# Kernel optimization log

Hardware: AMD Instinct MI355X
Metric: run time of the kernel (lower is better)

## Reference

```python
import jax, jax.numpy as jnp
import numpy as np

N_NODES = 50000
N_EDGES = 800000
HEADS = 4
OUT_CH = 64
NEG_SLOPE = 0.2  # PyG GATConv default


def gat_conv(x, edge_index, W, att_src, att_dst, bias):
    """PyG GATConv (concat=True, add_self_loops=True, eval mode).
    x: [N, F_in], edge_index: [2, E] (row 0 = src, row 1 = dst).
    W: [F_in, H*C], att_src/att_dst: [1, H, C], bias: [H*C].
    """
    n = x.shape[0]
    loops = jnp.arange(n, dtype=edge_index.dtype)
    src = jnp.concatenate([edge_index[0], loops])  # [E+N]
    dst = jnp.concatenate([edge_index[1], loops])

    h = (x @ W).reshape(n, HEADS, OUT_CH)           # [N, H, C]
    a_src = jnp.sum(h * att_src, axis=-1)           # [N, H]
    a_dst = jnp.sum(h * att_dst, axis=-1)           # [N, H]

    e = a_src[src] + a_dst[dst]                     # [E+N, H]
    e = jax.nn.leaky_relu(e, NEG_SLOPE)

    # segment softmax over incoming edges of each dst node
    e_max = jax.ops.segment_max(e, dst, num_segments=n)   # [N, H]
    e_exp = jnp.exp(e - e_max[dst])
    denom = jax.ops.segment_sum(e_exp, dst, num_segments=n)
    alpha = e_exp / (denom[dst] + 1e-16)            # [E+N, H]

    msg = h[src] * alpha[:, :, None]                # [E+N, H, C]
    out = jax.ops.segment_sum(msg, dst, num_segments=n)   # [N, H, C]
    return out.reshape(n, HEADS * OUT_CH) + bias


def setup_inputs() -> dict:
    key = jax.random.key(0)
    ks = jax.random.split(key, 10)
    d_in = 256
    d_hid = HEADS * OUT_CH  # 256
    s_in = 1.0 / np.sqrt(d_in)
    s_hid = 1.0 / np.sqrt(d_hid)
    return {
        "x": jax.random.normal(ks[0], (N_NODES, d_in), dtype=jnp.float32),
        "edge_index": jax.random.randint(ks[1], (2, N_EDGES), 0, N_NODES, dtype=jnp.int32),
        "W1": jax.random.normal(ks[2], (d_in, d_hid), dtype=jnp.float32) * s_in,
        "att_src1": jax.random.normal(ks[3], (1, HEADS, OUT_CH), dtype=jnp.float32) * s_hid,
        "att_dst1": jax.random.normal(ks[4], (1, HEADS, OUT_CH), dtype=jnp.float32) * s_hid,
        "b1": jnp.zeros((d_hid,), dtype=jnp.float32),
        "W2": jax.random.normal(ks[5], (d_hid, d_hid), dtype=jnp.float32) * s_hid,
        "att_src2": jax.random.normal(ks[6], (1, HEADS, OUT_CH), dtype=jnp.float32) * s_hid,
        "att_dst2": jax.random.normal(ks[7], (1, HEADS, OUT_CH), dtype=jnp.float32) * s_hid,
        "b2": jnp.zeros((d_hid,), dtype=jnp.float32),
    }


def reference(x, edge_index, W1, att_src1, att_dst1, b1, W2, att_src2, att_dst2, b2):
    # layer 1 + ELU (dropout is identity in eval mode)
    h = gat_conv(x, edge_index, W1, att_src1, att_dst1, b1)
    h = jax.nn.elu(h)
    # layer 2 + ELU
    h = gat_conv(h, edge_index, W2, att_src2, att_dst2, b2)
    h = jax.nn.elu(h)
    return h
```

## Files before the change

kernel.cpp:

```cpp
#include <hip/hip_runtime.h>
#include <hip/hip_bf16.h>

#define N_NODES 50000
#define N_EDGES 800000

typedef __attribute__((ext_vector_type(8))) short short8;
typedef __attribute__((ext_vector_type(4))) float floatx4;

__device__ __forceinline__ ushort f2bf(float f) {
    uint u = __float_as_uint(f);
    uint r = u + 0x7FFFu + ((u >> 16) & 1u);
    return (ushort)(r >> 16);
}
__device__ __forceinline__ float bfu2f(ushort h) {
    return __uint_as_float(((uint)h) << 16);
}
__device__ __forceinline__ float bflo(uint u) { return __uint_as_float(u << 16); }
__device__ __forceinline__ float bfhi(uint u) { return __uint_as_float(u & 0xffff0000u); }
__device__ __forceinline__ float lrelu(float e) { return e >= 0.f ? e : 0.2f * e; }

__global__ void deg_kernel(const int* __restrict__ dst, int* __restrict__ cnt, int E) {
    int i = blockIdx.x * blockDim.x + threadIdx.x;
    if (i < E) atomicAdd(&cnt[dst[i]], 1);
}

__global__ __launch_bounds__(256) void scan1_kernel(const int* __restrict__ cnt,
                                                    int* __restrict__ excl,
                                                    int* __restrict__ partial, int n) {
    __shared__ int sd[256];
    int tid = threadIdx.x;
    int i = blockIdx.x * 256 + tid;
    int v = (i < n) ? cnt[i] : 0;
    sd[tid] = v;
    __syncthreads();
    #pragma unroll
    for (int off = 1; off < 256; off <<= 1) {
        int t = (tid >= off) ? sd[tid - off] : 0;
        __syncthreads();
        sd[tid] += t;
        __syncthreads();
    }
    if (i < n) excl[i] = sd[tid] - v;
    if (tid == 255) partial[blockIdx.x] = sd[255];
}

__global__ __launch_bounds__(256) void scan2_kernel(int* __restrict__ partial, int nb) {
    __shared__ int sd[256];
    int tid = threadIdx.x;
    int v = (tid < nb) ? partial[tid] : 0;
    sd[tid] = v;
    __syncthreads();
    #pragma unroll
    for (int off = 1; off < 256; off <<= 1) {
        int t = (tid >= off) ? sd[tid - off] : 0;
        __syncthreads();
        sd[tid] += t;
        __syncthreads();
    }
    if (tid < nb) partial[tid] = sd[tid] - v;
}

__global__ __launch_bounds__(256) void scan3_kernel(const int* __restrict__ excl,
                                                    const int* __restrict__ partial,
                                                    int* __restrict__ row_ptr,
                                                    int* __restrict__ row_tmp, int n) {
    int i = blockIdx.x * 256 + threadIdx.x;
    if (i < n) {
        int v = excl[i] + partial[blockIdx.x];
        row_ptr[i] = v;
        row_tmp[i] = v;
    }
    if (i == 0) row_ptr[n] = N_EDGES;
}

__global__ void scatter_kernel(const int* __restrict__ src, const int* __restrict__ dst,
                               int* __restrict__ row_tmp, int* __restrict__ sorted_src, int E) {
    int i = blockIdx.x * blockDim.x + threadIdx.x;
    if (i < E) {
        int p = atomicAdd(&row_tmp[dst[i]], 1);
        sorted_src[p] = src[i];
    }
}

__global__ void prep_w(const float* __restrict__ W1, const float* __restrict__ W2,
                       ushort* __restrict__ Wt1_hi, ushort* __restrict__ Wt1_lo,
                       ushort* __restrict__ Wt2_hi, ushort* __restrict__ Wt2_lo) {
    int n = threadIdx.x, k = blockIdx.x & 255;
    const float* W = (blockIdx.x < 256) ? W1 : W2;
    ushort* Wh = (blockIdx.x < 256) ? Wt1_hi : Wt2_hi;
    ushort* Wl = (blockIdx.x < 256) ? Wt1_lo : Wt2_lo;
    float v = W[k * 256 + n];
    ushort hb = f2bf(v);
    Wh[n * 256 + k] = hb;
    Wl[n * 256 + k] = f2bf(v - bfu2f(hb));
}

__global__ __launch_bounds__(256) void gemm_att_kernel(const float* __restrict__ A,
                                                       const ushort* __restrict__ Wt_hi,
                                                       const ushort* __restrict__ Wt_lo,
                                                       const float* __restrict__ att_s,
                                                       const float* __restrict__ att_d,
                                                       ushort* __restrict__ H,
                                                       float* __restrict__ a_src,
                                                       float* __restrict__ a_dst, int M) {
    const int ROWP = 40;
    __shared__ ushort hi_s[256 * ROWP];
    __shared__ ushort lo_s[256 * ROWP];
    const int tid = threadIdx.x;
    const int wave = tid >> 6, lane = tid & 63;
    const int quad = lane >> 4, l16 = lane & 15;
    const int brow = blockIdx.x * 64;
    const int mrow = brow + wave * 16 + l16;
    const int mload = (mrow < M) ? mrow : (M - 1);

    floatx4 acc[16];
    #pragma unroll
    for (int t = 0; t < 16; t++) acc[t] = (floatx4){0.f, 0.f, 0.f, 0.f};

    for (int k0 = 0; k0 < 256; k0 += 32) {
        __syncthreads();
        {
            const ushort* gh = Wt_hi + tid * 256 + k0;
            const ushort* gl = Wt_lo + tid * 256 + k0;
            #pragma unroll
            for (int i = 0; i < 4; i++) {
                *reinterpret_cast<short8*>(&hi_s[tid * ROWP + i * 8]) =
                    *reinterpret_cast<const short8*>(gh + i * 8);
                *reinterpret_cast<short8*>(&lo_s[tid * ROWP + i * 8]) =
                    *reinterpret_cast<const short8*>(gl + i * 8);
            }
        }
        __syncthreads();
        const float* ap = A + (size_t)mload * 256 + k0 + quad * 8;
        float4 a0 = *reinterpret_cast<const float4*>(ap);
        float4 a1 = *reinterpret_cast<const float4*>(ap + 4);
        float av[8] = {a0.x, a0.y, a0.z, a0.w, a1.x, a1.y, a1.z, a1.w};
        short8 a_hi, a_lo;
        #pragma unroll
        for (int j = 0; j < 8; j++) {
            ushort hb = f2bf(av[j]);
            a_hi[j] = (short)hb;
            a_lo[j] = (short)f2bf(av[j] - bfu2f(hb));
        }
        #pragma unroll
        for (int t = 0; t < 16; t++) {
            int roff = (t * 16 + l16) * ROWP + quad * 8;
            short8 b_hi = *reinterpret_cast<const short8*>(&hi_s[roff]);
            short8 b_lo = *reinterpret_cast<const short8*>(&lo_s[roff]);
            acc[t] = __builtin_amdgcn_mfma_f32_16x16x32_bf16(a_hi, b_hi, acc[t], 0, 0, 0);
            acc[t] = __builtin_amdgcn_mfma_f32_16x16x32_bf16(a_hi, b_lo, acc[t], 0, 0, 0);
            acc[t] = __builtin_amdgcn_mfma_f32_16x16x32_bf16(a_lo, b_hi, acc[t], 0, 0, 0);
        }
    }
    float ps[4][4] = {}, pd[4][4] = {};
    #pragma unroll
    for (int t = 0; t < 16; t++) {
        int hh = t >> 2;
        float as_v = att_s[t * 16 + l16];
        float ad_v = att_d[t * 16 + l16];
        #pragma unroll
        for (int r = 0; r < 4; r++) {
            ps[hh][r] += acc[t][r] * as_v;
            pd[hh][r] += acc[t][r] * ad_v;
        }
    }
    #pragma unroll
    for (int off = 1; off < 16; off <<= 1) {
        #pragma unroll
        for (int hh = 0; hh < 4; hh++)
            #pragma unroll
            for (int r = 0; r < 4; r++) {
                ps[hh][r] += __shfl_xor(ps[hh][r], off, 64);
                pd[hh][r] += __shfl_xor(pd[hh][r], off, 64);
            }
    }
    if (l16 == 0) {
        #pragma unroll
        for (int r = 0; r < 4; r++) {
            int m = brow + wave * 16 + quad * 4 + r;
            if (m < M) {
                #pragma unroll
                for (int hh = 0; hh < 4; hh++) {
                    a_src[m * 4 + hh] = ps[hh][r];
                    a_dst[m * 4 + hh] = pd[hh][r];
                }
            }
        }
    }
    #pragma unroll
    for (int t = 0; t < 16; t++) {
        int col = t * 16 + l16;
        int c = col & 63, hh = col >> 6;
        #pragma unroll
        for (int r = 0; r < 4; r++) {
            int m = brow + wave * 16 + quad * 4 + r;
            if (m < M) H[(size_t)m * 256 + c * 4 + hh] = f2bf(acc[t][r]);
        }
    }
}

__global__ __launch_bounds__(256) void agg_kernel(const ushort* __restrict__ H,
                                                  const float* __restrict__ a_src,
                                                  const float* __restrict__ a_dst,
                                                  const int* __restrict__ row_ptr,
                                                  const int* __restrict__ sorted_src,
                                                  const float* __restrict__ bias,
                                                  float* __restrict__ out, int N) {
    int wave = threadIdx.x >> 6, lane = threadIdx.x & 63;
    int half = lane >> 5, hl = lane & 31;
    int i = blockIdx.x * 4 + wave;
    if (i >= N) return;
    float ad0 = a_dst[i * 4 + 0], ad1 = a_dst[i * 4 + 1];
    float ad2 = a_dst[i * 4 + 2], ad3 = a_dst[i * 4 + 3];
    float as0 = a_src[i * 4 + 0], as1 = a_src[i * 4 + 1];
    float as2 = a_src[i * 4 + 2], as3 = a_src[i * 4 + 3];
    float es0 = lrelu(as0 + ad0), es1 = lrelu(as1 + ad1);
    float es2 = lrelu(as2 + ad2), es3 = lrelu(as3 + ad3);
    float m0 = es0, m1 = es1, m2 = es2, m3 = es3;
    int start = row_ptr[i], end = row_ptr[i + 1];
    int deg = end - start;

    float a0 = 0.f, a1 = 0.f, a2 = 0.f, a3 = 0.f;
    float b0 = 0.f, b1 = 0.f, b2 = 0.f, b3 = 0.f;
    float dp0 = 0.f, dp1 = 0.f, dp2 = 0.f, dp3 = 0.f;

    if (deg <= 64) {
        float e0 = 0.f, e1 = 0.f, e2 = 0.f, e3 = 0.f;
        int s_lane = 0;
        if (lane < deg) {
            s_lane = sorted_src[start + lane];
            float4 av = *reinterpret_cast<const float4*>(a_src + (size_t)s_lane * 4);
            e0 = lrelu(av.x + ad0); e1 = lrelu(av.y + ad1);
            e2 = lrelu(av.z + ad2); e3 = lrelu(av.w + ad3);
            m0 = fmaxf(m0, e0); m1 = fmaxf(m1, e1);
            m2 = fmaxf(m2, e2); m3 = fmaxf(m3, e3);
        }
        #pragma unroll
        for (int off = 32; off; off >>= 1) {
            m0 = fmaxf(m0, __shfl_xor(m0, off, 64)); m1 = fmaxf(m1, __shfl_xor(m1, off, 64));
            m2 = fmaxf(m2, __shfl_xor(m2, off, 64)); m3 = fmaxf(m3, __shfl_xor(m3, off, 64));
        }
        float w0 = 0.f, w1 = 0.f, w2 = 0.f, w3 = 0.f;
        if (lane < deg) {
            w0 = __expf(e0 - m0); w1 = __expf(e1 - m1);
            w2 = __expf(e2 - m2); w3 = __expf(e3 - m3);
            dp0 = w0; dp1 = w1; dp2 = w2; dp3 = w3;
        }
        int npair = (deg + 1) >> 1;
        for (int t = 0; t < npair; t++) {
            int j = 2 * t + half;
            int sj = __shfl(s_lane, j, 64);
            float u0 = __shfl(w0, j, 64), u1 = __shfl(w1, j, 64);
            float u2 = __shfl(w2, j, 64), u3 = __shfl(w3, j, 64);
            uint4 hv = *reinterpret_cast<const uint4*>(H + (size_t)sj * 256 + hl * 8);
            a0 += u0 * bflo(hv.x); a1 += u1 * bfhi(hv.x);
            a2 += u2 * bflo(hv.y); a3 += u3 * bfhi(hv.y);
            b0 += u0 * bflo(hv.z); b1 += u1 * bfhi(hv.z);
            b2 += u2 * bflo(hv.w); b3 += u3 * bfhi(hv.w);
        }
    } else {
        for (int j = start + lane; j < end; j += 64) {
            int s = sorted_src[j];
            float4 av = *reinterpret_cast<const float4*>(a_src + (size_t)s * 4);
            m0 = fmaxf(m0, lrelu(av.x + ad0)); m1 = fmaxf(m1, lrelu(av.y + ad1));
            m2 = fmaxf(m2, lrelu(av.z + ad2)); m3 = fmaxf(m3, lrelu(av.w + ad3));
        }
        #pragma unroll
        for (int off = 32; off; off >>= 1) {
            m0 = fmaxf(m0, __shfl_xor(m0, off, 64)); m1 = fmaxf(m1, __shfl_xor(m1, off, 64));
            m2 = fmaxf(m2, __shfl_xor(m2, off, 64)); m3 = fmaxf(m3, __shfl_xor(m3, off, 64));
        }
        for (int c0 = start; c0 < end; c0 += 64) {
            int nc = min(64, end - c0);
            float w0 = 0.f, w1 = 0.f, w2 = 0.f, w3 = 0.f;
            int sl = 0;
            if (lane < nc) {
                sl = sorted_src[c0 + lane];
                float4 av = *reinterpret_cast<const float4*>(a_src + (size_t)sl * 4);
                w0 = __expf(lrelu(av.x + ad0) - m0); w1 = __expf(lrelu(av.y + ad1) - m1);
                w2 = __expf(lrelu(av.z + ad2) - m2); w3 = __expf(lrelu(av.w + ad3) - m3);
                dp0 += w0; dp1 += w1; dp2 += w2; dp3 += w3;
            }
            int npair = (nc + 1) >> 1;
            for (int t = 0; t < npair; t++) {
                int j = 2 * t + half;
                int sj = __shfl(sl, j, 64);
                float u0 = __shfl(w0, j, 64), u1 = __shfl(w1, j, 64);
                float u2 = __shfl(w2, j, 64), u3 = __shfl(w3, j, 64);
                uint4 hv = *reinterpret_cast<const uint4*>(H + (size_t)sj * 256 + hl * 8);
                a0 += u0 * bflo(hv.x); a1 += u1 * bfhi(hv.x);
                a2 += u2 * bflo(hv.y); a3 += u3 * bfhi(hv.y);
                b0 += u0 * bflo(hv.z); b1 += u1 * bfhi(hv.z);
                b2 += u2 * bflo(hv.w); b3 += u3 * bfhi(hv.w);
            }
        }
    }
    a0 += __shfl_xor(a0, 32, 64); a1 += __shfl_xor(a1, 32, 64);
    a2 += __shfl_xor(a2, 32, 64); a3 += __shfl_xor(a3, 32, 64);
    b0 += __shfl_xor(b0, 32, 64); b1 += __shfl_xor(b1, 32, 64);
    b2 += __shfl_xor(b2, 32, 64); b3 += __shfl_xor(b3, 32, 64);
    #pragma unroll
    for (int off = 32; off; off >>= 1) {
        dp0 += __shfl_xor(dp0, off, 64); dp1 += __shfl_xor(dp1, off, 64);
        dp2 += __shfl_xor(dp2, off, 64); dp3 += __shfl_xor(dp3, off, 64);
    }
    float ws0 = __expf(es0 - m0), ws1 = __expf(es1 - m1);
    float ws2 = __expf(es2 - m2), ws3 = __expf(es3 - m3);
    {
        uint4 hv = *reinterpret_cast<const uint4*>(H + (size_t)i * 256 + hl * 8);
        a0 += ws0 * bflo(hv.x); a1 += ws1 * bfhi(hv.x);
        a2 += ws2 * bflo(hv.y); a3 += ws3 * bfhi(hv.y);
        b0 += ws0 * bflo(hv.z); b1 += ws1 * bfhi(hv.z);
        b2 += ws2 * bflo(hv.w); b3 += ws3 * bfhi(hv.w);
    }
    if (half == 0) {
        float r0 = 1.f / (dp0 + ws0 + 1e-16f), r1 = 1.f / (dp1 + ws1 + 1e-16f);
        float r2 = 1.f / (dp2 + ws2 + 1e-16f), r3 = 1.f / (dp3 + ws3 + 1e-16f);
        float2 o;
        float* op = out + (size_t)i * 256 + hl * 2;
        float v;
        v = a0 * r0 + bias[2 * hl];       o.x = (v > 0.f) ? v : expm1f(v);
        v = b0 * r0 + bias[2 * hl + 1];   o.y = (v > 0.f) ? v : expm1f(v);
        *reinterpret_cast<float2*>(op) = o;
        v = a1 * r1 + bias[64 + 2 * hl];     o.x = (v > 0.f) ? v : expm1f(v);
        v = b1 * r1 + bias[64 + 2 * hl + 1]; o.y = (v > 0.f) ? v : expm1f(v);
        *reinterpret_cast<float2*>(op + 64) = o;
        v = a2 * r2 + bias[128 + 2 * hl];     o.x = (v > 0.f) ? v : expm1f(v);
        v = b2 * r2 + bias[128 + 2 * hl + 1]; o.y = (v > 0.f) ? v : expm1f(v);
        *reinterpret_cast<float2*>(op + 128) = o;
        v = a3 * r3 + bias[192 + 2 * hl];     o.x = (v > 0.f) ? v : expm1f(v);
        v = b3 * r3 + bias[192 + 2 * hl + 1]; o.y = (v > 0.f) ? v : expm1f(v);
        *reinterpret_cast<float2*>(op + 192) = o;
    }
}

extern "C" void kernel_launch(void* const* d_in, const int* in_sizes, int n_in,
                              void* d_out, int out_size, void* d_ws, size_t ws_size,
                              hipStream_t stream) {
    const float* x      = (const float*)d_in[0];
    const int*   eidx   = (const int*)d_in[1];
    const float* W1     = (const float*)d_in[2];
    const float* att_s1 = (const float*)d_in[3];
    const float* att_d1 = (const float*)d_in[4];
    const float* b1     = (const float*)d_in[5];
    const float* W2     = (const float*)d_in[6];
    const float* att_s2 = (const float*)d_in[7];
    const float* att_d2 = (const float*)d_in[8];
    const float* b2     = (const float*)d_in[9];
    float* out = (float*)d_out;

    const int N = N_NODES, E = N_EDGES;
    char* ws = (char*)d_ws;
    size_t off = 0;
    auto alloc = [&](size_t bytes) -> void* {
        void* p = ws + off;
        off += (bytes + 255) & ~(size_t)255;
        return p;
    };
    ushort* h       = (ushort*)alloc((size_t)N * 256 * sizeof(ushort));
    float*  a_src   = (float*) alloc((size_t)N * 4 * sizeof(float));
    float*  a_dst   = (float*) alloc((size_t)N * 4 * sizeof(float));
    int*    cnt     = (int*)   alloc((size_t)N * sizeof(int));
    int*    row_ptr = (int*)   alloc((size_t)(N + 1) * sizeof(int));
    int*    row_tmp = (int*)   alloc((size_t)N * sizeof(int));
    int*    sorted  = (int*)   alloc((size_t)E * sizeof(int));
    int*    excl    = (int*)   alloc((size_t)N * sizeof(int));
    int*    partial = (int*)   alloc(256 * sizeof(int));
    ushort* Wt1_hi  = (ushort*)alloc(256 * 256 * sizeof(ushort));
    ushort* Wt1_lo  = (ushort*)alloc(256 * 256 * sizeof(ushort));
    ushort* Wt2_hi  = (ushort*)alloc(256 * 256 * sizeof(ushort));
    ushort* Wt2_lo  = (ushort*)alloc(256 * 256 * sizeof(ushort));
    float*  x2      = out;
    (void)ws_size; (void)in_sizes; (void)n_in; (void)out_size;

    const int* e_src = eidx;
    const int* e_dst = eidx + E;
    const int nsb = (N + 255) / 256;

    prep_w<<<512, 256, 0, stream>>>(W1, W2, Wt1_hi, Wt1_lo, Wt2_hi, Wt2_lo);
    hipMemsetAsync(cnt, 0, N * sizeof(int), stream);
    deg_kernel<<<(E + 255) / 256, 256, 0, stream>>>(e_dst, cnt, E);
    scan1_kernel<<<nsb, 256, 0, stream>>>(cnt, excl, partial, N);
    scan2_kernel<<<1, 256, 0, stream>>>(partial, nsb);
    scan3_kernel<<<nsb, 256, 0, stream>>>(excl, partial, row_ptr, row_tmp, N);
    scatter_kernel<<<(E + 255) / 256, 256, 0, stream>>>(e_src, e_dst, row_tmp, sorted, E);

    int gblk = (N + 63) / 64;
    int nblk = (N + 3) / 4;
    gemm_att_kernel<<<gblk, 256, 0, stream>>>(x, Wt1_hi, Wt1_lo, att_s1, att_d1,
                                              h, a_src, a_dst, N);
    agg_kernel<<<nblk, 256, 0, stream>>>(h, a_src, a_dst, row_ptr, sorted, b1, x2, N);
    gemm_att_kernel<<<gblk, 256, 0, stream>>>(x2, Wt2_hi, Wt2_lo, att_s2, att_d2,
                                              h, a_src, a_dst, N);
    agg_kernel<<<nblk, 256, 0, stream>>>(h, a_src, a_dst, row_ptr, sorted, b2, out, N);
}
```

Measured before the change: 500.9 us.

## Precompute per-edge softmax weights without max and split GEMM columns across grid

Adds a per-edge kernel that computes exp(leaky_relu(a_src+a_dst)) for every sorted edge, using a new sorted_dst array written during the CSR scatter. The aggregation kernel drops the segment-max pass and the shuffle broadcast, and streams the precomputed weights with H rows. The unnormalized exp risks overflow on large logits. The GEMM is also split into two column halves via blockIdx.y to halve LDS and accumulators for more occupancy, and the final store now uses both half-waves.

```diff
diff --git a/kernel.cpp b/kernel.cpp
--- a/kernel.cpp
+++ b/kernel.cpp
@@ -74,11 +74,14 @@
 }
 
 __global__ void scatter_kernel(const int* __restrict__ src, const int* __restrict__ dst,
-                               int* __restrict__ row_tmp, int* __restrict__ sorted_src, int E) {
+                               int* __restrict__ row_tmp, int* __restrict__ sorted_src,
+                               int* __restrict__ sorted_dst, int E) {
     int i = blockIdx.x * blockDim.x + threadIdx.x;
     if (i < E) {
-        int p = atomicAdd(&row_tmp[dst[i]], 1);
+        int d = dst[i];
+        int p = atomicAdd(&row_tmp[d], 1);
         sorted_src[p] = src[i];
+        sorted_dst[p] = d;
     }
 }
 
@@ -104,31 +107,30 @@
                                                        float* __restrict__ a_src,
                                                        float* __restrict__ a_dst, int M) {
     const int ROWP = 40;
-    __shared__ ushort hi_s[256 * ROWP];
-    __shared__ ushort lo_s[256 * ROWP];
+    __shared__ ushort hi_s[128 * ROWP];
+    __shared__ ushort lo_s[128 * ROWP];
     const int tid = threadIdx.x;
     const int wave = tid >> 6, lane = tid & 63;
     const int quad = lane >> 4, l16 = lane & 15;
     const int brow = blockIdx.x * 64;
+    const int coff = blockIdx.y * 128;
     const int mrow = brow + wave * 16 + l16;
     const int mload = (mrow < M) ? mrow : (M - 1);
 
-    floatx4 acc[16];
-    #pragma unroll
-    for (int t = 0; t < 16; t++) acc[t] = (floatx4){0.f, 0.f, 0.f, 0.f};
+    floatx4 acc[8];
+    #pragma unroll
+    for (int t = 0; t < 8; t++) acc[t] = (floatx4){0.f, 0.f, 0.f, 0.f};
 
     for (int k0 = 0; k0 < 256; k0 += 32) {
         __syncthreads();
         {
-            const ushort* gh = Wt_hi + tid * 256 + k0;
-            const ushort* gl = Wt_lo + tid * 256 + k0;
+            int t = tid & 127;
+            const ushort* g = ((tid < 128) ? Wt_hi : Wt_lo) + (size_t)(coff + t) * 256 + k0;
+            ushort* d = ((tid < 128) ? hi_s : lo_s) + t * ROWP;
             #pragma unroll
-            for (int i = 0; i < 4; i++) {
-                *reinterpret_cast<short8*>(&hi_s[tid * ROWP + i * 8]) =
-                    *reinterpret_cast<const short8*>(gh + i * 8);
-                *reinterpret_cast<short8*>(&lo_s[tid * ROWP + i * 8]) =
-                    *reinterpret_cast<const short8*>(gl + i * 8);
-            }
+            for (int i = 0; i < 4; i++)
+                *reinterpret_cast<short8*>(d + i * 8) =
+                    *reinterpret_cast<const short8*>(g + i * 8);
         }
         __syncthreads();
         const float* ap = A + (size_t)mload * 256 + k0 + quad * 8;
@@ -143,7 +145,7 @@
             a_lo[j] = (short)f2bf(av[j] - bfu2f(hb));
         }
         #pragma unroll
-        for (int t = 0; t < 16; t++) {
+        for (int t = 0; t < 8; t++) {
             int roff = (t * 16 + l16) * ROWP + quad * 8;
             short8 b_hi = *reinterpret_cast<const short8*>(&hi_s[roff]);
             short8 b_lo = *reinterpret_cast<const short8*>(&lo_s[roff]);
@@ -152,12 +154,13 @@
             acc[t] = __builtin_amdgcn_mfma_f32_16x16x32_bf16(a_lo, b_hi, acc[t], 0, 0, 0);
         }
     }
-    float ps[4][4] = {}, pd[4][4] = {};
-    #pragma unroll
-    for (int t = 0; t < 16; t++) {
+    const int hb = blockIdx.y * 2;
+    float ps[2][4] = {}, pd[2][4] = {};
+    #pragma unroll
+    for (int t = 0; t < 8; t++) {
         int hh = t >> 2;
-        float as_v = att_s[t * 16 + l16];
-        float ad_v = att_d[t * 16 + l16];
+        float as_v = att_s[coff + t * 16 + l16];
+        float ad_v = att_d[coff + t * 16 + l16];
         #pragma unroll
         for (int r = 0; r < 4; r++) {
             ps[hh][r] += acc[t][r] * as_v;
@@ -167,7 +170,7 @@
     #pragma unroll
     for (int off = 1; off < 16; off <<= 1) {
         #pragma unroll
-        for (int hh = 0; hh < 4; hh++)
+        for (int hh = 0; hh < 2; hh++)
             #pragma unroll
             for (int r = 0; r < 4; r++) {
                 ps[hh][r] += __shfl_xor(ps[hh][r], off, 64);
@@ -180,16 +183,16 @@
             int m = brow + wave * 16 + quad * 4 + r;
             if (m < M) {
                 #pragma unroll
-                for (int hh = 0; hh < 4; hh++) {
-                    a_src[m * 4 + hh] = ps[hh][r];
-                    a_dst[m * 4 + hh] = pd[hh][r];
+                for (int hh = 0; hh < 2; hh++) {
+                    a_src[m * 4 + hb + hh] = ps[hh][r];
+                    a_dst[m * 4 + hb + hh] = pd[hh][r];
                 }
             }
         }
     }
     #pragma unroll
-    for (int t = 0; t < 16; t++) {
-        int col = t * 16 + l16;
+    for (int t = 0; t < 8; t++) {
+        int col = coff + t * 16 + l16;
         int c = col & 63, hh = col >> 6;
         #pragma unroll
         for (int r = 0; r < 4; r++) {
@@ -197,6 +200,24 @@
             if (m < M) H[(size_t)m * 256 + c * 4 + hh] = f2bf(acc[t][r]);
         }
     }
+}
+
+__global__ __launch_bounds__(256) void ew_kernel(const float* __restrict__ a_src,
+                                                 const float* __restrict__ a_dst,
+                                                 const int* __restrict__ sorted_src,
+                                                 const int* __restrict__ sorted_dst,
+                                                 float* __restrict__ ew, int E) {
+    int j = blockIdx.x * 256 + threadIdx.x;
+    if (j >= E) return;
+    int s = sorted_src[j], d = sorted_dst[j];
+    float4 as_ = *reinterpret_cast<const float4*>(a_src + (size_t)s * 4);
+    float4 ad_ = *reinterpret_cast<const float4*>(a_dst + (size_t)d * 4);
+    float4 w;
+    w.x = __expf(lrelu(as_.x + ad_.x));
+    w.y = __expf(lrelu(as_.y + ad_.y));
+    w.z = __expf(lrelu(as_.z + ad_.z));
+    w.w = __expf(lrelu(as_.w + ad_.w));
+    *reinterpret_cast<float4*>(ew + (size_t)j * 4) = w;
 }
 
 __global__ __launch_bounds__(256) void agg_kernel(const ushort* __restrict__ H,
@@ -204,108 +225,39 @@
                                                   const float* __restrict__ a_dst,
                                                   const int* __restrict__ row_ptr,
                                                   const int* __restrict__ sorted_src,
+                                                  const float* __restrict__ ew,
                                                   const float* __restrict__ bias,
                                                   float* __restrict__ out, int N) {
     int wave = threadIdx.x >> 6, lane = threadIdx.x & 63;
     int half = lane >> 5, hl = lane & 31;
     int i = blockIdx.x * 4 + wave;
     if (i >= N) return;
-    float ad0 = a_dst[i * 4 + 0], ad1 = a_dst[i * 4 + 1];
-    float ad2 = a_dst[i * 4 + 2], ad3 = a_dst[i * 4 + 3];
-    float as0 = a_src[i * 4 + 0], as1 = a_src[i * 4 + 1];
-    float as2 = a_src[i * 4 + 2], as3 = a_src[i * 4 + 3];
-    float es0 = lrelu(as0 + ad0), es1 = lrelu(as1 + ad1);
-    float es2 = lrelu(as2 + ad2), es3 = lrelu(as3 + ad3);
-    float m0 = es0, m1 = es1, m2 = es2, m3 = es3;
+    float4 asv = *reinterpret_cast<const float4*>(a_src + (size_t)i * 4);
+    float4 adv = *reinterpret_cast<const float4*>(a_dst + (size_t)i * 4);
+    float ws0 = __expf(lrelu(asv.x + adv.x)), ws1 = __expf(lrelu(asv.y + adv.y));
+    float ws2 = __expf(lrelu(asv.z + adv.z)), ws3 = __expf(lrelu(asv.w + adv.w));
     int start = row_ptr[i], end = row_ptr[i + 1];
-    int deg = end - start;
 
     float a0 = 0.f, a1 = 0.f, a2 = 0.f, a3 = 0.f;
     float b0 = 0.f, b1 = 0.f, b2 = 0.f, b3 = 0.f;
     float dp0 = 0.f, dp1 = 0.f, dp2 = 0.f, dp3 = 0.f;
 
-    if (deg <= 64) {
-        float e0 = 0.f, e1 = 0.f, e2 = 0.f, e3 = 0.f;
-        int s_lane = 0;
-        if (lane < deg) {
-            s_lane = sorted_src[start + lane];
-            float4 av = *reinterpret_cast<const float4*>(a_src + (size_t)s_lane * 4);
-            e0 = lrelu(av.x + ad0); e1 = lrelu(av.y + ad1);
-            e2 = lrelu(av.z + ad2); e3 = lrelu(av.w + ad3);
-            m0 = fmaxf(m0, e0); m1 = fmaxf(m1, e1);
-            m2 = fmaxf(m2, e2); m3 = fmaxf(m3, e3);
-        }
-        #pragma unroll
-        for (int off = 32; off; off >>= 1) {
-            m0 = fmaxf(m0, __shfl_xor(m0, off, 64)); m1 = fmaxf(m1, __shfl_xor(m1, off, 64));
-            m2 = fmaxf(m2, __shfl_xor(m2, off, 64)); m3 = fmaxf(m3, __shfl_xor(m3, off, 64));
-        }
-        float w0 = 0.f, w1 = 0.f, w2 = 0.f, w3 = 0.f;
-        if (lane < deg) {
-            w0 = __expf(e0 - m0); w1 = __expf(e1 - m1);
-            w2 = __expf(e2 - m2); w3 = __expf(e3 - m3);
-            dp0 = w0; dp1 = w1; dp2 = w2; dp3 = w3;
-        }
-        int npair = (deg + 1) >> 1;
-        for (int t = 0; t < npair; t++) {
-            int j = 2 * t + half;
-            int sj = __shfl(s_lane, j, 64);
-            float u0 = __shfl(w0, j, 64), u1 = __shfl(w1, j, 64);
-            float u2 = __shfl(w2, j, 64), u3 = __shfl(w3, j, 64);
-            uint4 hv = *reinterpret_cast<const uint4*>(H + (size_t)sj * 256 + hl * 8);
-            a0 += u0 * bflo(hv.x); a1 += u1 * bfhi(hv.x);
-            a2 += u2 * bflo(hv.y); a3 += u3 * bfhi(hv.y);
-            b0 += u0 * bflo(hv.z); b1 += u1 * bfhi(hv.z);
-            b2 += u2 * bflo(hv.w); b3 += u3 * bfhi(hv.w);
-        }
-    } else {
-        for (int j = start + lane; j < end; j += 64) {
-            int s = sorted_src[j];
-            float4 av = *reinterpret_cast<const float4*>(a_src + (size_t)s * 4);
-            m0 = fmaxf(m0, lrelu(av.x + ad0)); m1 = fmaxf(m1, lrelu(av.y + ad1));
-            m2 = fmaxf(m2, lrelu(av.z + ad2)); m3 = fmaxf(m3, lrelu(av.w + ad3));
-        }
-        #pragma unroll
-        for (int off = 32; off; off >>= 1) {
-            m0 = fmaxf(m0, __shfl_xor(m0, off, 64)); m1 = fmaxf(m1, __shfl_xor(m1, off, 64));
-            m2 = fmaxf(m2, __shfl_xor(m2, off, 64)); m3 = fmaxf(m3, __shfl_xor(m3, off, 64));
-        }
-        for (int c0 = start; c0 < end; c0 += 64) {
-            int nc = min(64, end - c0);
-            float w0 = 0.f, w1 = 0.f, w2 = 0.f, w3 = 0.f;
-            int sl = 0;
-            if (lane < nc) {
-                sl = sorted_src[c0 + lane];
-                float4 av = *reinterpret_cast<const float4*>(a_src + (size_t)sl * 4);
-                w0 = __expf(lrelu(av.x + ad0) - m0); w1 = __expf(lrelu(av.y + ad1) - m1);
-                w2 = __expf(lrelu(av.z + ad2) - m2); w3 = __expf(lrelu(av.w + ad3) - m3);
-                dp0 += w0; dp1 += w1; dp2 += w2; dp3 += w3;
-            }
-            int npair = (nc + 1) >> 1;
-            for (int t = 0; t < npair; t++) {
-                int j = 2 * t + half;
-                int sj = __shfl(sl, j, 64);
-                float u0 = __shfl(w0, j, 64), u1 = __shfl(w1, j, 64);
-                float u2 = __shfl(w2, j, 64), u3 = __shfl(w3, j, 64);
-                uint4 hv = *reinterpret_cast<const uint4*>(H + (size_t)sj * 256 + hl * 8);
-                a0 += u0 * bflo(hv.x); a1 += u1 * bfhi(hv.x);
-                a2 += u2 * bflo(hv.y); a3 += u3 * bfhi(hv.y);
-                b0 += u0 * bflo(hv.z); b1 += u1 * bfhi(hv.z);
-                b2 += u2 * bflo(hv.w); b3 += u3 * bfhi(hv.w);
-            }
-        }
+    for (int j = start + half; j < end; j += 2) {
+        int sj = sorted_src[j];
+        float4 w = *reinterpret_cast<const float4*>(ew + (size_t)j * 4);
+        uint4 hv = *reinterpret_cast<const uint4*>(H + (size_t)sj * 256 + hl * 8);
+        a0 += w.x * bflo(hv.x); a1 += w.y * bfhi(hv.x);
+        a2 += w.z * bflo(hv.y); a3 += w.w * bfhi(hv.y);
+        b0 += w.x * bflo(hv.z); b1 += w.y * bfhi(hv.z);
+        b2 += w.z * bflo(hv.w); b3 += w.w * bfhi(hv.w);
+        dp0 += w.x; dp1 += w.y; dp2 += w.z; dp3 += w.w;
     }
     a0 += __shfl_xor(a0, 32, 64); a1 += __shfl_xor(a1, 32, 64);
     a2 += __shfl_xor(a2, 32, 64); a3 += __shfl_xor(a3, 32, 64);
     b0 += __shfl_xor(b0, 32, 64); b1 += __shfl_xor(b1, 32, 64);
     b2 += __shfl_xor(b2, 32, 64); b3 += __shfl_xor(b3, 32, 64);
-    #pragma unroll
-    for (int off = 32; off; off >>= 1) {
-        dp0 += __shfl_xor(dp0, off, 64); dp1 += __shfl_xor(dp1, off, 64);
-        dp2 += __shfl_xor(dp2, off, 64); dp3 += __shfl_xor(dp3, off, 64);
-    }
-    float ws0 = __expf(es0 - m0), ws1 = __expf(es1 - m1);
-    float ws2 = __expf(es2 - m2), ws3 = __expf(es3 - m3);
+    dp0 += __shfl_xor(dp0, 32, 64); dp1 += __shfl_xor(dp1, 32, 64);
+    dp2 += __shfl_xor(dp2, 32, 64); dp3 += __shfl_xor(dp3, 32, 64);
     {
         uint4 hv = *reinterpret_cast<const uint4*>(H + (size_t)i * 256 + hl * 8);
         a0 += ws0 * bflo(hv.x); a1 += ws1 * bfhi(hv.x);
@@ -313,25 +265,22 @@
         b0 += ws0 * bflo(hv.z); b1 += ws1 * bfhi(hv.z);
         b2 += ws2 * bflo(hv.w); b3 += ws3 * bfhi(hv.w);
     }
-    if (half == 0) {
-        float r0 = 1.f / (dp0 + ws0 + 1e-16f), r1 = 1.f / (dp1 + ws1 + 1e-16f);
-        float r2 = 1.f / (dp2 + ws2 + 1e-16f), r3 = 1.f / (dp3 + ws3 + 1e-16f);
-        float2 o;
-        float* op = out + (size_t)i * 256 + hl * 2;
-        float v;
-        v = a0 * r0 + bias[2 * hl];       o.x = (v > 0.f) ? v : expm1f(v);
-        v = b0 * r0 + bias[2 * hl + 1];   o.y = (v > 0.f) ? v : expm1f(v);
-        *reinterpret_cast<float2*>(op) = o;
-        v = a1 * r1 + bias[64 + 2 * hl];     o.x = (v > 0.f) ? v : expm1f(v);
-        v = b1 * r1 + bias[64 + 2 * hl + 1]; o.y = (v > 0.f) ? v : expm1f(v);
-        *reinterpret_cast<float2*>(op + 64) = o;
-        v = a2 * r2 + bias[128 + 2 * hl];     o.x = (v > 0.f) ? v : expm1f(v);
-        v = b2 * r2 + bias[128 + 2 * hl + 1]; o.y = (v > 0.f) ? v : expm1f(v);
-        *reinterpret_cast<float2*>(op + 128) = o;
-        v = a3 * r3 + bias[192 + 2 * hl];     o.x = (v > 0.f) ? v : expm1f(v);
-        v = b3 * r3 + bias[192 + 2 * hl + 1]; o.y = (v > 0.f) ? v : expm1f(v);
-        *reinterpret_cast<float2*>(op + 192) = o;
-    }
+    float r0 = 1.f / (dp0 + ws0 + 1e-16f), r1 = 1.f / (dp1 + ws1 + 1e-16f);
+    float r2 = 1.f / (dp2 + ws2 + 1e-16f), r3 = 1.f / (dp3 + ws3 + 1e-16f);
+    float* op = out + (size_t)i * 256 + hl * 2;
+    float va = (half == 0) ? a0 : a2, vb = (half == 0) ? b0 : b2;
+    float ra = (half == 0) ? r0 : r2;
+    float va2 = (half == 0) ? a1 : a3, vb2 = (half == 0) ? b1 : b3;
+    float ra2 = (half == 0) ? r1 : r3;
+    int hofs = half * 128;
+    float2 o;
+    float v;
+    v = va * ra + bias[hofs + 2 * hl];      o.x = (v > 0.f) ? v : expm1f(v);
+    v = vb * ra + bias[hofs + 2 * hl + 1];  o.y = (v > 0.f) ? v : expm1f(v);
+    *reinterpret_cast<float2*>(op + hofs) = o;
+    v = va2 * ra2 + bias[hofs + 64 + 2 * hl];     o.x = (v > 0.f) ? v : expm1f(v);
+    v = vb2 * ra2 + bias[hofs + 64 + 2 * hl + 1]; o.y = (v > 0.f) ? v : expm1f(v);
+    *reinterpret_cast<float2*>(op + hofs + 64) = o;
 }
 
 extern "C" void kernel_launch(void* const* d_in, const int* in_sizes, int n_in,
@@ -358,12 +307,14 @@
         return p;
     };
     ushort* h       = (ushort*)alloc((size_t)N * 256 * sizeof(ushort));
+    float*  ew      = (float*) alloc((size_t)E * 4 * sizeof(float));
     float*  a_src   = (float*) alloc((size_t)N * 4 * sizeof(float));
     float*  a_dst   = (float*) alloc((size_t)N * 4 * sizeof(float));
     int*    cnt     = (int*)   alloc((size_t)N * sizeof(int));
     int*    row_ptr = (int*)   alloc((size_t)(N + 1) * sizeof(int));
     int*    row_tmp = (int*)   alloc((size_t)N * sizeof(int));
     int*    sorted  = (int*)   alloc((size_t)E * sizeof(int));
+    int*    sortedd = (int*)   alloc((size_t)E * sizeof(int));
     int*    excl    = (int*)   alloc((size_t)N * sizeof(int));
     int*    partial = (int*)   alloc(256 * sizeof(int));
     ushort* Wt1_hi  = (ushort*)alloc(256 * 256 * sizeof(ushort));
@@ -376,21 +327,24 @@
     const int* e_src = eidx;
     const int* e_dst = eidx + E;
     const int nsb = (N + 255) / 256;
+    const int neb = (E + 255) / 256;
 
     prep_w<<<512, 256, 0, stream>>>(W1, W2, Wt1_hi, Wt1_lo, Wt2_hi, Wt2_lo);
     hipMemsetAsync(cnt, 0, N * sizeof(int), stream);
-    deg_kernel<<<(E + 255) / 256, 256, 0, stream>>>(e_dst, cnt, E);
+    deg_kernel<<<neb, 256, 0, stream>>>(e_dst, cnt, E);
     scan1_kernel<<<nsb, 256, 0, stream>>>(cnt, excl, partial, N);
     scan2_kernel<<<1, 256, 0, stream>>>(partial, nsb);
     scan3_kernel<<<nsb, 256, 0, stream>>>(excl, partial, row_ptr, row_tmp, N);
-    scatter_kernel<<<(E + 255) / 256, 256, 0, stream>>>(e_src, e_dst, row_tmp, sorted, E);
-
-    int gblk = (N + 63) / 64;
+    scatter_kernel<<<neb, 256, 0, stream>>>(e_src, e_dst, row_tmp, sorted, sortedd, E);
+
+    dim3 ggrid((N + 63) / 64, 2);
     int nblk = (N + 3) / 4;
-    gemm_att_kernel<<<gblk, 256, 0, stream>>>(x, Wt1_hi, Wt1_lo, att_s1, att_d1,
-                                              h, a_src, a_dst, N);
-    agg_kernel<<<nblk, 256, 0, stream>>>(h, a_src, a_dst, row_ptr, sorted, b1, x2, N);
-    gemm_att_kernel<<<gblk, 256, 0, stream>>>(x2, Wt2_hi, Wt2_lo, att_s2, att_d2,
-                                              h, a_src, a_dst, N);
-    agg_kernel<<<nblk, 256, 0, stream>>>(h, a_src, a_dst, row_ptr, sorted, b2, out, N);
-}
+    gemm_att_kernel<<<ggrid, 256, 0, stream>>>(x, Wt1_hi, Wt1_lo, att_s1, att_d1,
+                                               h, a_src, a_dst, N);
+    ew_kernel<<<neb, 256, 0, stream>>>(a_src, a_dst, sorted, sortedd, ew, E);
+    agg_kernel<<<nblk, 256, 0, stream>>>(h, a_src, a_dst, row_ptr, sorted, ew, b1, x2, N);
+    gemm_att_kernel<<<ggrid, 256, 0, stream>>>(x2, Wt2_hi, Wt2_lo, att_s2, att_d2,
+                                               h, a_src, a_dst, N);
+    ew_kernel<<<neb, 256, 0, stream>>>(a_src, a_dst, sorted, sortedd, ew, E);
+    agg_kernel<<<nblk, 256, 0, stream>>>(h, a_src, a_dst, row_ptr, sorted, ew, b2, out, N);
+}
```

Result: faster. 475.3 us (-5.1%).
